# Kernel optimization log

Hardware: AMD Instinct MI355X
Metric: run time of the kernel (lower is better)

Reference implementation:

```python
import math
import jax, jax.numpy as jnp
import numpy as np

B, N = 1, 512
C_S, C_Z, H, C, P_Q, P_V = 384, 128, 12, 16, 4, 8
CAT = C_Z * H + C * H + 3 * H * P_V + 1  # 2017


def _apply(t_r, t_t, x):
    # t_r: (b,n,3,3), t_t: (b,n,3), x: (b,3,h,p,n) -> global frame coords
    xg = jnp.einsum('bnij,bjhpn->bihpn', t_r, x)
    return xg + jnp.swapaxes(t_t, 1, 2)[:, :, None, None, :]


def setup_inputs() -> dict:
    key = jax.random.key(0)
    ks = jax.random.split(key, 14)
    f = lambda k, shp: jax.random.normal(k, shp, dtype=jnp.float32)
    return {
        's': f(ks[0], (B, C_S, N)),
        'z': f(ks[1], (B, C_Z, N, N)),
        't_r': f(ks[2], (B, N, 3, 3)),
        't_t': f(ks[3], (B, N, 3)),
        'Wq': f(ks[4], (C * H, C_S)) * 0.02,
        'Wk': f(ks[5], (C * H, C_S)) * 0.02,
        'Wv': f(ks[6], (C * H, C_S)) * 0.02,
        'Wqp': f(ks[7], (3 * H * P_Q, C_S)) * 0.02,
        'Wkp': f(ks[8], (3 * H * P_Q, C_S)) * 0.02,
        'Wvp': f(ks[9], (3 * H * P_V, C_S)) * 0.02,
        'Wb': f(ks[10], (H, C_Z)) * 0.02,
        'gamma': f(ks[11], (H, 1, 1)) * 0.5,
        'Ws': f(ks[12], (C_S, CAT)) * 0.02,
        'bs': jnp.zeros((C_S,), dtype=jnp.float32),
    }


def reference(s, z, t_r, t_t, Wq, Wk, Wv, Wqp, Wkp, Wvp, Wb, gamma, Ws, bs):
    b, _, n = s.shape
    w_c = math.sqrt(2.0 / (9.0 * P_Q))
    w_l = math.sqrt(1.0 / 3.0)

    proj = lambda W: jnp.einsum('oc,bcn->bon', W, s)
    # torch rearrange 'b (c h) i -> b c h i' == reshape(b, c, h, n)
    q = proj(Wq).reshape(b, C, H, n)
    k = proj(Wk).reshape(b, C, H, n)
    v = proj(Wv).reshape(b, C, H, n)
    qp = proj(Wqp).reshape(b, 3, H, P_Q, n)
    kp = proj(Wkp).reshape(b, 3, H, P_Q, n)
    vp = proj(Wvp).reshape(b, 3, H, P_V, n)

    qg = _apply(t_r, t_t, qp)  # (b,3,h,p,n)
    kg = _apply(t_r, t_t, kp)
    diff = qg[..., :, None] - kg[..., None, :]          # (b,3,h,p,n,n)
    dist2 = jnp.sum(diff * diff, axis=(1, 3))           # sum coords + points -> (b,h,n,n)
    tmp = jax.nn.softplus(gamma)[None] * (w_c / 2.0) * dist2

    b_bias = jnp.einsum('hc,bcij->bhij', Wb, z)
    qk = jnp.einsum('bchi,bchj->bhij', q, k) / math.sqrt(C)
    a = jax.nn.softmax(w_l * (qk + b_bias - tmp), axis=-1)  # (b,h,n,n)

    o1 = jnp.einsum('bhij,bcij->bchi', a, z).reshape(b, C_Z * H, n)
    o2 = jnp.einsum('bhij,bchj->bchi', a, v).reshape(b, C * H, n)

    vg = _apply(t_r, t_t, vp)                           # (b,3,h,pv,n)
    o3g = jnp.einsum('bhij,bchpj->bchpi', a, vg)        # (b,3,h,pv,n)
    t_r_inv = jnp.swapaxes(t_r, -1, -2)
    t_t_inv = jnp.einsum('bnij,bnj->bni', -t_r_inv, t_t)
    o3 = _apply(t_r_inv, t_t_inv, o3g).reshape(b, 3 * H * P_V, n)
    o3_norm = jnp.linalg.norm(o3, axis=1, keepdims=True)  # (b,1,n)

    cat = jnp.concatenate([o1, o2, o3, o3_norm], axis=1)  # (b, CAT, n)
    return jnp.einsum('oc,bcn->bon', Ws, cat) + bs[None, :, None]
```

## Files before the change

### kernel.cpp

```cpp
#include <hip/hip_runtime.h>
#include <math.h>

#define N 512
#define H 12
#define CC 16
#define CZ 128
#define CS 384
#define PQ 4
#define PV 8
#define CATR 2017

__global__ __launch_bounds__(256) void k_proj(
    const float* __restrict__ s,
    const float* __restrict__ Wq, const float* __restrict__ Wk, const float* __restrict__ Wv,
    const float* __restrict__ Wqp, const float* __restrict__ Wkp, const float* __restrict__ Wvp,
    float* __restrict__ proj)
{
    __shared__ float Wt[16][33];
    __shared__ float St[32][128];
    int t = threadIdx.x;
    int o0 = blockIdx.x * 16;
    int n0 = blockIdx.y * 128;
    const float* Wsrc; int orow;
    if (o0 < 192)      { Wsrc = Wq;  orow = o0; }
    else if (o0 < 384) { Wsrc = Wk;  orow = o0-192; }
    else if (o0 < 576) { Wsrc = Wv;  orow = o0-384; }
    else if (o0 < 720) { Wsrc = Wqp; orow = o0-576; }
    else if (o0 < 864) { Wsrc = Wkp; orow = o0-720; }
    else               { Wsrc = Wvp; orow = o0-864; }

    int og = t >> 6, nl = t & 63;
    float acc[4][2] = {};
    for (int c0 = 0; c0 < CS; c0 += 32) {
        __syncthreads();
        for (int k = 0; k < 2; k++) {
            int idx = t + k*256;
            int oo = idx >> 5, ccol = idx & 31;
            Wt[oo][ccol] = Wsrc[(orow+oo)*CS + c0 + ccol];
        }
        for (int k = 0; k < 4; k++) {
            int idx = t + k*256;
            int ccr = idx >> 5, nn4 = idx & 31;
            float4 v = *(const float4*)&s[(c0+ccr)*N + n0 + nn4*4];
            *(float4*)&St[ccr][nn4*4] = v;
        }
        __syncthreads();
        for (int kk = 0; kk < 32; kk++) {
            float sv0 = St[kk][nl], sv1 = St[kk][nl+64];
            #pragma unroll
            for (int r = 0; r < 4; r++) {
                float w = Wt[og*4+r][kk];
                acc[r][0] += w * sv0;
                acc[r][1] += w * sv1;
            }
        }
    }
    for (int r = 0; r < 4; r++) {
        int o = o0 + og*4 + r;
        proj[o*N + n0 + nl]      = acc[r][0];
        proj[o*N + n0 + 64 + nl] = acc[r][1];
    }
}

__global__ void k_frames(const float* __restrict__ proj,
                         const float* __restrict__ t_r, const float* __restrict__ t_t,
                         float* __restrict__ qg, float* __restrict__ kg, float* __restrict__ vg)
{
    int gid = blockIdx.x * blockDim.x + threadIdx.x;
    int n = gid & (N-1);
    int hp = gid >> 9;
    if (hp >= 192) return;
    const float* src; float* dst; int rowb, stride;
    if (hp < 48)      { src = proj + 576*N; dst = qg; rowb = hp;    stride = 48; }
    else if (hp < 96) { src = proj + 720*N; dst = kg; rowb = hp-48; stride = 48; }
    else              { src = proj + 864*N; dst = vg; rowb = hp-96; stride = 96; }
    float x0 = src[(rowb + 0*stride)*N + n];
    float x1 = src[(rowb + 1*stride)*N + n];
    float x2 = src[(rowb + 2*stride)*N + n];
    #pragma unroll
    for (int d = 0; d < 3; d++) {
        float r0 = t_r[(n*3+d)*3+0], r1 = t_r[(n*3+d)*3+1], r2 = t_r[(n*3+d)*3+2];
        dst[(rowb + d*stride)*N + n] = r0*x0 + r1*x1 + r2*x2 + t_t[n*3+d];
    }
}

__global__ __launch_bounds__(512, 4) void k_logits(
    const float* __restrict__ z, const float* __restrict__ proj,
    const float* __restrict__ qg, const float* __restrict__ kg,
    const float* __restrict__ Wb, const float* __restrict__ gamma,
    float* __restrict__ a)
{
    __shared__ float pm[12][8];
    __shared__ float ps[12][8];
    const int i = blockIdx.x;
    const int t = threadIdx.x;
    const int w = t >> 6;
    const int l = t & 63;
    const size_t NN = (size_t)N * N;
    const float w_l  = 0.57735026918962584f;
    const float w_c2 = 0.11785113019775793f;

    float ch[12];
    #pragma unroll
    for (int h = 0; h < 12; ++h) {
        float g = gamma[h];
        float sp = (g > 20.f) ? g : log1pf(expf(g));
        ch[h] = sp * w_c2;
    }

    float acc[12] = {};

    {
        const float* zp = z + (size_t)i*N + t;
        for (int c0 = 0; c0 < CZ; c0 += 16) {
            float zb[16];
            #pragma unroll
            for (int u = 0; u < 16; ++u) zb[u] = zp[(size_t)(c0+u)*NN];
            #pragma unroll
            for (int h = 0; h < 12; ++h)
                #pragma unroll
                for (int u = 0; u < 16; ++u)
                    acc[h] = fmaf(Wb[h*CZ + c0 + u], zb[u], acc[h]);
        }
    }
    {
        const float* qq = proj;
        const float* kk = proj + 192*N;
        for (int c = 0; c < 16; ++c) {
            float kv[12];
            #pragma unroll
            for (int h = 0; h < 12; ++h)
                kv[h] = kk[(size_t)(c*12+h)*N + t];
            #pragma unroll
            for (int h = 0; h < 12; ++h)
                acc[h] = fmaf(0.25f * qq[(size_t)(c*12+h)*N + i], kv[h], acc[h]);
        }
    }
    float k2[12] = {}, q2[12] = {};
    for (int dp = 0; dp < 12; ++dp) {
        int d = dp >> 2, p = dp & 3;
        #pragma unroll
        for (int h = 0; h < 12; ++h) {
            int r = (d*12 + h)*4 + p;
            float kv = kg[(size_t)r*N + t];
            float qv = qg[(size_t)r*N + i];
            acc[h] = fmaf(2.f*ch[h]*qv, kv, acc[h]);
            k2[h]  = fmaf(kv, kv, k2[h]);
            q2[h]  = fmaf(qv, qv, q2[h]);
        }
    }

    float lv[12], mw[12];
    #pragma unroll
    for (int h = 0; h < 12; ++h)
        lv[h] = w_l * (acc[h] - ch[h]*(q2[h] + k2[h]));

    #pragma unroll
    for (int h = 0; h < 12; ++h) {
        float m = lv[h];
        for (int s = 32; s; s >>= 1) m = fmaxf(m, __shfl_xor(m, s));
        float e = __expf(lv[h] - m);
        float sm = e;
        for (int s = 32; s; s >>= 1) sm += __shfl_xor(sm, s);
        lv[h] = e; mw[h] = m;
        if (l == 0) { pm[h][w] = m; ps[h][w] = sm; }
    }
    __syncthreads();
    #pragma unroll
    for (int h = 0; h < 12; ++h) {
        float mg = pm[h][0];
        #pragma unroll
        for (int u = 1; u < 8; ++u) mg = fmaxf(mg, pm[h][u]);
        float sg = 0.f;
        #pragma unroll
        for (int u = 0; u < 8; ++u) sg += ps[h][u] * __expf(pm[h][u] - mg);
        float f = __expf(mw[h] - mg) / sg;
        a[((size_t)h*N + i)*N + t] = lv[h] * f;
    }
}

__global__ __launch_bounds__(256, 8) void k_o1(
    const float* __restrict__ a, const float* __restrict__ z,
    float* __restrict__ o1T)
{
    __shared__ float zls[64*36];
    __shared__ float als[12][36];
    const int i  = blockIdx.x;
    const int c0 = blockIdx.y * 64;
    const int t  = threadIdx.x;
    const int cg = t & 31, hg = (t >> 5) & 1, jq = t >> 6;

    float acc[2][6] = {};
    for (int jc = 0; jc < 16; ++jc) {
        __syncthreads();
        #pragma unroll
        for (int k = 0; k < 2; ++k) {
            int idx = t + k*256;
            int c = idx >> 3, j4 = idx & 7;
            *(float4*)&zls[c*36 + j4*4] =
                *(const float4*)&z[((size_t)(c0+c)*N + i)*N + jc*32 + j4*4];
        }
        if (t < 96) {
            int h = t >> 3, j4 = t & 7;
            *(float4*)&als[h][j4*4] =
                *(const float4*)&a[((size_t)h*N + i)*N + jc*32 + j4*4];
        }
        __syncthreads();
        #pragma unroll
        for (int s = 0; s < 2; ++s) {
            int jo = jq*8 + s*4;
            float4 a4[6];
            #pragma unroll
            for (int hh = 0; hh < 6; ++hh)
                a4[hh] = *(const float4*)&als[hg*6+hh][jo];
            #pragma unroll
            for (int r = 0; r < 2; ++r) {
                float4 z4 = *(const float4*)&zls[(cg + 32*r)*36 + jo];
                #pragma unroll
                for (int hh = 0; hh < 6; ++hh)
                    acc[r][hh] += z4.x*a4[hh].x + z4.y*a4[hh].y
                                + z4.z*a4[hh].z + z4.w*a4[hh].w;
            }
        }
    }
    const int sl = t & 63;
    __syncthreads();
    if (jq >= 2) {
        float* rb = &zls[(jq-2)*832 + sl*13];
        #pragma unroll
        for (int r = 0; r < 2; ++r)
            #pragma unroll
            for (int hh = 0; hh < 6; ++hh) rb[r*6+hh] = acc[r][hh];
    }
    __syncthreads();
    if (jq < 2) {
        const float* rb = &zls[jq*832 + sl*13];
        #pragma unroll
        for (int r = 0; r < 2; ++r)
            #pragma unroll
            for (int hh = 0; hh < 6; ++hh) acc[r][hh] += rb[r*6+hh];
    }
    __syncthreads();
    if (jq == 1) {
        float* rb = &zls[sl*13];
        #pragma unroll
        for (int r = 0; r < 2; ++r)
            #pragma unroll
            for (int hh = 0; hh < 6; ++hh) rb[r*6+hh] = acc[r][hh];
    }
    __syncthreads();
    if (jq == 0) {
        const float* rb = &zls[sl*13];
        #pragma unroll
        for (int r = 0; r < 2; ++r)
            #pragma unroll
            for (int hh = 0; hh < 3; ++hh) {
                int c = c0 + cg + 32*r, h = hg*6 + hh*2;
                float2 v2;
                v2.x = acc[r][hh*2]   + rb[r*6+hh*2];
                v2.y = acc[r][hh*2+1] + rb[r*6+hh*2+1];
                *(float2*)&o1T[(size_t)i*1536 + c*12 + h] = v2;
            }
    }
}

__global__ __launch_bounds__(256) void k_o2o3g(
    const float* __restrict__ a, const float* __restrict__ proj, const float* __restrict__ vg,
    float* __restrict__ catB, float* __restrict__ o3g)
{
    __shared__ float ats[8*132];
    __shared__ float vts[40*132];
    int h = blockIdx.x, i0 = blockIdx.y*8;
    int t = threadIdx.x;
    int il = t & 7, rg = (t>>3)&7, jq = t>>6;
    const float* v = proj + 384*N;
    float acc[5] = {};
    for (int jc = 0; jc < 4; jc++) {
        __syncthreads();
        {
            int ii = t >> 5, j4 = t & 31;
            *(float4*)&ats[ii*132 + j4*4] =
                *(const float4*)&a[((size_t)h*N + i0+ii)*N + jc*128 + j4*4];
        }
        #pragma unroll
        for (int k = 0; k < 5; k++) {
            int idx = t + k*256;
            int r = idx >> 5, j4 = idx & 31;
            const float* src = (r < 16) ? (v + (size_t)(r*H + h)*N)
                : (vg + (size_t)(((r-16)>>3)*96 + h*PV + ((r-16)&7))*N);
            *(float4*)&vts[r*132 + j4*4] = *(const float4*)&src[jc*128 + j4*4];
        }
        __syncthreads();
        #pragma unroll
        for (int s = 0; s < 8; s++) {
            int jo = jq*32 + s*4;
            float4 a4 = *(const float4*)&ats[il*132 + jo];
            #pragma unroll
            for (int r = 0; r < 5; r++) {
                float4 v4 = *(const float4*)&vts[(rg*5+r)*132 + jo];
                acc[r] += v4.x*a4.x + v4.y*a4.y + v4.z*a4.z + v4.w*a4.w;
            }
        }
    }
    __syncthreads();
    if (jq >= 2) {
        float* rb = &ats[((jq-2)*64 + (t & 63))*5];
        #pragma unroll
        for (int r = 0; r < 5; r++) rb[r] = acc[r];
    }
    __syncthreads();
    if (jq < 2) {
        const float* rb = &ats[(jq*64 + (t & 63))*5];
        #pragma unroll
        for (int r = 0; r < 5; r++) acc[r] += rb[r];
        if (jq == 1) {
            float* rb2 = &ats[640 + (t & 63)*5];
            #pragma unroll
            for (int r = 0; r < 5; r++) rb2[r] = acc[r];
        }
    }
    __syncthreads();
    if (jq == 0) {
        const float* rb2 = &ats[640 + t*5];
        #pragma unroll
        for (int r = 0; r < 5; r++) {
            float val = acc[r] + rb2[r];
            int row = rg*5 + r;
            if (row < 16) catB[(size_t)(row*H + h)*N + i0 + il] = val;
            else { int rr = row - 16;
                   o3g[(size_t)((rr>>3)*96 + h*PV + (rr&7))*N + i0 + il] = val; }
        }
    }
}

__global__ void k_o3(const float* __restrict__ o3g,
                     const float* __restrict__ t_r, const float* __restrict__ t_t,
                     float* __restrict__ catB)
{
    int gid = blockIdx.x*blockDim.x + threadIdx.x;
    int i = gid & (N-1), hp = gid >> 9;
    if (hp >= 96) return;
    float x0 = o3g[(size_t)(0*96 + hp)*N + i] - t_t[i*3+0];
    float x1 = o3g[(size_t)(1*96 + hp)*N + i] - t_t[i*3+1];
    float x2 = o3g[(size_t)(2*96 + hp)*N + i] - t_t[i*3+2];
    #pragma unroll
    for (int d = 0; d < 3; d++) {
        float o = t_r[(i*3+0)*3+d]*x0 + t_r[(i*3+1)*3+d]*x1 + t_r[(i*3+2)*3+d]*x2;
        catB[(size_t)(192 + d*96 + hp)*N + i] = o;
    }
}

__global__ void k_norm(float* __restrict__ catB)
{
    __shared__ float red[8][32];
    int il = threadIdx.x & 31, g = threadIdx.x >> 5;
    int i = blockIdx.x*32 + il;
    float acc = 0.f;
    for (int r = g*36; r < g*36 + 36; ++r) {
        float v = catB[(size_t)(192+r)*N + i];
        acc += v*v;
    }
    red[g][il] = acc;
    __syncthreads();
    if (g == 0) {
        acc = 0.f;
        #pragma unroll
        for (int u = 0; u < 8; ++u) acc += red[u][il];
        catB[(size_t)480*N + i] = sqrtf(acc);
    }
}

__global__ __launch_bounds__(256) void k_final(
    const float* __restrict__ Ws, const float* __restrict__ bs,
    const float* __restrict__ o1T, const float* __restrict__ catB,
    float* __restrict__ out)
{
    __shared__ float Wt[16*33];
    __shared__ float Ct[32*66];
    int o0 = blockIdx.x*16, n0 = blockIdx.y*64;
    int ks = blockIdx.z;
    int kbeg = ks*512, kend = min(CATR, kbeg+512);
    int t = threadIdx.x;
    int og = t >> 6, nl = t & 63;
    float acc[4] = {};
    for (int c0 = kbeg; c0 < kend; c0 += 32) {
        __syncthreads();
        for (int k = 0; k < 2; k++) {
            int idx = t + k*256;
            int oo = idx >> 5, ccol = idx & 31;
            int c = c0 + ccol;
            Wt[oo*33 + ccol] = (c < kend) ? Ws[(size_t)(o0+oo)*CATR + c] : 0.f;
        }
        if (ks < 3) {
            for (int k = 0; k < 2; k++) {
                int idx = t + k*256;
                int nn = idx >> 3, c4 = idx & 7;
                float4 v = *(const float4*)&o1T[(size_t)(n0+nn)*1536 + c0 + c4*4];
                Ct[(c4*4+0)*66 + nn] = v.x;
                Ct[(c4*4+1)*66 + nn] = v.y;
                Ct[(c4*4+2)*66 + nn] = v.z;
                Ct[(c4*4+3)*66 + nn] = v.w;
            }
        } else {
            for (int k = 0; k < 4; k++) {
                int idx = t + k*256;
                int ccr = idx >> 5, j2 = idx & 31;
                int c = c0 + ccr;
                float2 vv; vv.x = 0.f; vv.y = 0.f;
                if (c < kend) vv = *(const float2*)&catB[(size_t)(c-1536)*N + n0 + j2*2];
                *(float2*)&Ct[ccr*66 + j2*2] = vv;
            }
        }
        __syncthreads();
        int klim = min(32, kend - c0);
        for (int kk = 0; kk < klim; kk++) {
            float cv = Ct[kk*66 + nl];
            #pragma unroll
            for (int r = 0; r < 4; r++)
                acc[r] += Wt[(og*4+r)*33 + kk] * cv;
        }
    }
    #pragma unroll
    for (int r = 0; r < 4; r++) {
        int o = o0 + og*4 + r;
        float val = acc[r];
        if (ks == 0) val += bs[o];
        atomicAdd(&out[(size_t)o*N + n0 + nl], val);
    }
}

extern "C" void kernel_launch(void* const* d_in, const int* in_sizes, int n_in,
                              void* d_out, int out_size, void* d_ws, size_t ws_size,
                              hipStream_t stream)
{
    const float* s     = (const float*)d_in[0];
    const float* z     = (const float*)d_in[1];
    const float* t_r   = (const float*)d_in[2];
    const float* t_t   = (const float*)d_in[3];
    const float* Wq    = (const float*)d_in[4];
    const float* Wk    = (const float*)d_in[5];
    const float* Wv    = (const float*)d_in[6];
    const float* Wqp   = (const float*)d_in[7];
    const float* Wkp   = (const float*)d_in[8];
    const float* Wvp   = (const float*)d_in[9];
    const float* Wb    = (const float*)d_in[10];
    const float* gamma = (const float*)d_in[11];
    const float* Ws    = (const float*)d_in[12];
    const float* bs    = (const float*)d_in[13];
    float* out = (float*)d_out;

    float* ws   = (float*)d_ws;
    float* proj = ws;
    float* qg   = proj + 1152*N;
    float* kg   = qg   + 144*N;
    float* vg   = kg   + 144*N;
    float* o3g  = vg   + 288*N;
    float* a    = o3g  + 288*N;
    float* o1T  = a    + (size_t)H*N*N;
    float* catB = o1T  + (size_t)N*1536;

    k_proj   <<<dim3(72,4),   256, 0, stream>>>(s, Wq, Wk, Wv, Wqp, Wkp, Wvp, proj);
    k_frames <<<384,          256, 0, stream>>>(proj, t_r, t_t, qg, kg, vg);
    k_logits <<<512,          512, 0, stream>>>(z, proj, qg, kg, Wb, gamma, a);
    k_o1     <<<dim3(512,2),  256, 0, stream>>>(a, z, o1T);
    k_o2o3g  <<<dim3(12,64),  256, 0, stream>>>(a, proj, vg, catB, o3g);
    k_o3     <<<192,          256, 0, stream>>>(o3g, t_r, t_t, catB);
    k_norm   <<<16,           256, 0, stream>>>(catB);
    hipMemsetAsync(out, 0, (size_t)CS*N*sizeof(float), stream);
    k_final  <<<dim3(24,8,4), 256, 0, stream>>>(Ws, bs, o1T, catB, out);
}
```

Measured before the change: 391.6 us.

## Stage z through double-buffered LDS with float4 loads in logits kernel

The z-bias reduction in k_logits now loads z tiles of 16 channels with float4 global loads into a double-buffered shared-memory tile, so the next tile's load overlaps the FMAs on the current one. Wb is transposed into LDS and read as float4 vectors. The 0.25 q-scaling moves into the projection kernel, and the qk and point-distance loops are regrouped into 24-wide batches. The roughly 70KB of LDS per block can lower occupancy below the four blocks requested, and the extra barriers add sync cost.

```diff
diff --git a/kernel.cpp b/kernel.cpp
--- a/kernel.cpp
+++ b/kernel.cpp
@@ -55,10 +55,11 @@
             }
         }
     }
+    float scale = (o0 < 192) ? 0.25f : 1.0f;
     for (int r = 0; r < 4; r++) {
         int o = o0 + og*4 + r;
-        proj[o*N + n0 + nl]      = acc[r][0];
-        proj[o*N + n0 + 64 + nl] = acc[r][1];
+        proj[o*N + n0 + nl]      = scale * acc[r][0];
+        proj[o*N + n0 + 64 + nl] = scale * acc[r][1];
     }
 }
 
@@ -90,6 +91,8 @@
     const float* __restrict__ Wb, const float* __restrict__ gamma,
     float* __restrict__ a)
 {
+    __shared__ float zt[2][16*512];
+    __shared__ float WbT[CZ*12];
     __shared__ float pm[12][8];
     __shared__ float ps[12][8];
     const int i = blockIdx.x;
@@ -100,53 +103,90 @@
     const float w_l  = 0.57735026918962584f;
     const float w_c2 = 0.11785113019775793f;
 
-    float ch[12];
+    for (int idx = t; idx < 12*CZ; idx += 512) {
+        int h = idx >> 7, c = idx & 127;
+        WbT[c*12 + h] = Wb[idx];
+    }
+
+    float ch[12], ch2[12];
     #pragma unroll
     for (int h = 0; h < 12; ++h) {
         float g = gamma[h];
         float sp = (g > 20.f) ? g : log1pf(expf(g));
         ch[h] = sp * w_c2;
+        ch2[h] = 2.f * ch[h];
     }
 
     float acc[12] = {};
 
     {
-        const float* zp = z + (size_t)i*N + t;
-        for (int c0 = 0; c0 < CZ; c0 += 16) {
-            float zb[16];
-            #pragma unroll
-            for (int u = 0; u < 16; ++u) zb[u] = zp[(size_t)(c0+u)*NN];
-            #pragma unroll
-            for (int h = 0; h < 12; ++h)
+        const float* kk = proj + 192*N;
+        const float* qq = proj;
+        for (int cb = 0; cb < 8; ++cb) {
+            float kv[24];
+            #pragma unroll
+            for (int u = 0; u < 24; ++u)
+                kv[u] = kk[(size_t)(cb*24+u)*N + t];
+            #pragma unroll
+            for (int u = 0; u < 24; ++u) {
+                int h = u % 12;
+                acc[h] = fmaf(qq[(size_t)(cb*24+u)*N + i], kv[u], acc[h]);
+            }
+        }
+    }
+    float k2[12] = {}, q2[12] = {};
+    for (int db = 0; db < 6; ++db) {
+        float kv[24];
+        #pragma unroll
+        for (int u = 0; u < 24; ++u) {
+            int dp = db*2 + (u/12); int d = dp >> 2, p = dp & 3; int h = u % 12;
+            kv[u] = kg[(size_t)(d*48 + h*4 + p)*N + t];
+        }
+        #pragma unroll
+        for (int u = 0; u < 24; ++u) {
+            int dp = db*2 + (u/12); int d = dp >> 2, p = dp & 3; int h = u % 12;
+            float qv = qg[(size_t)(d*48 + h*4 + p)*N + i];
+            acc[h] = fmaf(ch2[h]*qv, kv[u], acc[h]);
+            k2[h]  = fmaf(kv[u], kv[u], k2[h]);
+            q2[h]  = fmaf(qv, qv, q2[h]);
+        }
+    }
+
+    {
+        const int zc = t >> 5;
+        const int zj = (t & 31) * 4;
+        const float* zsrc = z + (size_t)zc*NN + (size_t)i*N + zj;
+        float4 g[4];
+        #pragma unroll
+        for (int k = 0; k < 4; ++k) g[k] = *(const float4*)(zsrc + k*128);
+        #pragma unroll
+        for (int k = 0; k < 4; ++k) *(float4*)&zt[0][zc*512 + zj + k*128] = g[k];
+        #pragma unroll
+        for (int k = 0; k < 4; ++k) g[k] = *(const float4*)(zsrc + 16*NN + k*128);
+        __syncthreads();
+        for (int tb = 0; tb < 8; ++tb) {
+            #pragma unroll
+            for (int c = 0; c < 16; ++c) {
+                float zv = zt[tb & 1][c*512 + t];
+                float wbv[12];
+                *(float4*)&wbv[0] = *(const float4*)&WbT[(tb*16+c)*12 + 0];
+                *(float4*)&wbv[4] = *(const float4*)&WbT[(tb*16+c)*12 + 4];
+                *(float4*)&wbv[8] = *(const float4*)&WbT[(tb*16+c)*12 + 8];
                 #pragma unroll
-                for (int u = 0; u < 16; ++u)
-                    acc[h] = fmaf(Wb[h*CZ + c0 + u], zb[u], acc[h]);
-        }
-    }
-    {
-        const float* qq = proj;
-        const float* kk = proj + 192*N;
-        for (int c = 0; c < 16; ++c) {
-            float kv[12];
-            #pragma unroll
-            for (int h = 0; h < 12; ++h)
-                kv[h] = kk[(size_t)(c*12+h)*N + t];
-            #pragma unroll
-            for (int h = 0; h < 12; ++h)
-                acc[h] = fmaf(0.25f * qq[(size_t)(c*12+h)*N + i], kv[h], acc[h]);
-        }
-    }
-    float k2[12] = {}, q2[12] = {};
-    for (int dp = 0; dp < 12; ++dp) {
-        int d = dp >> 2, p = dp & 3;
-        #pragma unroll
-        for (int h = 0; h < 12; ++h) {
-            int r = (d*12 + h)*4 + p;
-            float kv = kg[(size_t)r*N + t];
-            float qv = qg[(size_t)r*N + i];
-            acc[h] = fmaf(2.f*ch[h]*qv, kv, acc[h]);
-            k2[h]  = fmaf(kv, kv, k2[h]);
-            q2[h]  = fmaf(qv, qv, q2[h]);
+                for (int h = 0; h < 12; ++h)
+                    acc[h] = fmaf(wbv[h], zv, acc[h]);
+            }
+            if (tb < 7) {
+                #pragma unroll
+                for (int k = 0; k < 4; ++k)
+                    *(float4*)&zt[(tb+1) & 1][zc*512 + zj + k*128] = g[k];
+                if (tb < 6) {
+                    #pragma unroll
+                    for (int k = 0; k < 4; ++k)
+                        g[k] = *(const float4*)(zsrc + (size_t)(tb+2)*16*NN + k*128);
+                }
+            }
+            __syncthreads();
         }
     }
 
```

Result: slower. 716.7 us (+83.0%).

## Stage z bias tiles through shared memory with register prefetch in logits kernel

Applied to the files above, without the earlier changes.

The logits kernel now loads z for row i into a 16-channel shared-memory tile using float4 loads, prefetching the next tile into registers while computing the pair-bias FMAs from LDS. The z pass moves after the qk and point-distance terms, and the 1/sqrt(C) query scale is folded into the projection kernel's store. The intent is wider global loads and latency hiding on the dominant z read. In exchange it adds 32KB of LDS per block, extra barriers, and drops the occupancy hint from the launch bounds, which may reduce resident blocks.

```diff
diff --git a/kernel.cpp b/kernel.cpp
--- a/kernel.cpp
+++ b/kernel.cpp
@@ -55,10 +55,11 @@
             }
         }
     }
+    float scale = (o0 < 192) ? 0.25f : 1.0f;
     for (int r = 0; r < 4; r++) {
         int o = o0 + og*4 + r;
-        proj[o*N + n0 + nl]      = acc[r][0];
-        proj[o*N + n0 + 64 + nl] = acc[r][1];
+        proj[o*N + n0 + nl]      = scale * acc[r][0];
+        proj[o*N + n0 + 64 + nl] = scale * acc[r][1];
     }
 }
 
@@ -84,12 +85,13 @@
     }
 }
 
-__global__ __launch_bounds__(512, 4) void k_logits(
+__global__ __launch_bounds__(512) void k_logits(
     const float* __restrict__ z, const float* __restrict__ proj,
     const float* __restrict__ qg, const float* __restrict__ kg,
     const float* __restrict__ Wb, const float* __restrict__ gamma,
     float* __restrict__ a)
 {
+    __shared__ float zt[16*512];
     __shared__ float pm[12][8];
     __shared__ float ps[12][8];
     const int i = blockIdx.x;
@@ -111,19 +113,6 @@
     float acc[12] = {};
 
     {
-        const float* zp = z + (size_t)i*N + t;
-        for (int c0 = 0; c0 < CZ; c0 += 16) {
-            float zb[16];
-            #pragma unroll
-            for (int u = 0; u < 16; ++u) zb[u] = zp[(size_t)(c0+u)*NN];
-            #pragma unroll
-            for (int h = 0; h < 12; ++h)
-                #pragma unroll
-                for (int u = 0; u < 16; ++u)
-                    acc[h] = fmaf(Wb[h*CZ + c0 + u], zb[u], acc[h]);
-        }
-    }
-    {
         const float* qq = proj;
         const float* kk = proj + 192*N;
         for (int c = 0; c < 16; ++c) {
@@ -133,27 +122,71 @@
                 kv[h] = kk[(size_t)(c*12+h)*N + t];
             #pragma unroll
             for (int h = 0; h < 12; ++h)
-                acc[h] = fmaf(0.25f * qq[(size_t)(c*12+h)*N + i], kv[h], acc[h]);
-        }
-    }
-    float k2[12] = {}, q2[12] = {};
-    for (int dp = 0; dp < 12; ++dp) {
-        int d = dp >> 2, p = dp & 3;
-        #pragma unroll
-        for (int h = 0; h < 12; ++h) {
-            int r = (d*12 + h)*4 + p;
-            float kv = kg[(size_t)r*N + t];
-            float qv = qg[(size_t)r*N + i];
-            acc[h] = fmaf(2.f*ch[h]*qv, kv, acc[h]);
-            k2[h]  = fmaf(kv, kv, k2[h]);
-            q2[h]  = fmaf(qv, qv, q2[h]);
+                acc[h] = fmaf(qq[(size_t)(c*12+h)*N + i], kv[h], acc[h]);
+        }
+    }
+    {
+        float k2[12] = {}, q2[12] = {};
+        for (int dp = 0; dp < 12; ++dp) {
+            int d = dp >> 2, p = dp & 3;
+            #pragma unroll
+            for (int h = 0; h < 12; ++h) {
+                int r = (d*12 + h)*4 + p;
+                float kv = kg[(size_t)r*N + t];
+                float qv = qg[(size_t)r*N + i];
+                acc[h] = fmaf(2.f*ch[h]*qv, kv, acc[h]);
+                k2[h]  = fmaf(kv, kv, k2[h]);
+                q2[h]  = fmaf(qv, qv, q2[h]);
+            }
+        }
+        #pragma unroll
+        for (int h = 0; h < 12; ++h)
+            acc[h] = fmaf(-ch[h], k2[h] + q2[h], acc[h]);
+    }
+
+    {
+        const int zc = t >> 5;
+        const int zj = (t & 31) * 4;
+        const float* zsrc = z + (size_t)zc*NN + (size_t)i*N + zj;
+        float4 g0 = *(const float4*)(zsrc);
+        float4 g1 = *(const float4*)(zsrc + 128);
+        float4 g2 = *(const float4*)(zsrc + 256);
+        float4 g3 = *(const float4*)(zsrc + 384);
+        *(float4*)&zt[zc*512 + zj]       = g0;
+        *(float4*)&zt[zc*512 + zj + 128] = g1;
+        *(float4*)&zt[zc*512 + zj + 256] = g2;
+        *(float4*)&zt[zc*512 + zj + 384] = g3;
+        __syncthreads();
+        for (int tb = 0; tb < 8; ++tb) {
+            if (tb < 7) {
+                const float* zn = zsrc + (size_t)(tb+1)*16*NN;
+                g0 = *(const float4*)(zn);
+                g1 = *(const float4*)(zn + 128);
+                g2 = *(const float4*)(zn + 256);
+                g3 = *(const float4*)(zn + 384);
+            }
+            #pragma unroll
+            for (int c = 0; c < 16; ++c) {
+                float zv = zt[c*512 + t];
+                #pragma unroll
+                for (int h = 0; h < 12; ++h)
+                    acc[h] = fmaf(Wb[h*CZ + tb*16 + c], zv, acc[h]);
+            }
+            __syncthreads();
+            if (tb < 7) {
+                *(float4*)&zt[zc*512 + zj]       = g0;
+                *(float4*)&zt[zc*512 + zj + 128] = g1;
+                *(float4*)&zt[zc*512 + zj + 256] = g2;
+                *(float4*)&zt[zc*512 + zj + 384] = g3;
+                __syncthreads();
+            }
         }
     }
 
     float lv[12], mw[12];
     #pragma unroll
     for (int h = 0; h < 12; ++h)
-        lv[h] = w_l * (acc[h] - ch[h]*(q2[h] + k2[h]));
+        lv[h] = w_l * acc[h];
 
     #pragma unroll
     for (int h = 0; h < 12; ++h) {
```

New measurement: 390.0 us. About the same (-0.4%).
